# Kernel tuning notes

Hardware: AMD Instinct MI355X
Metric: run time of the kernel (lower is better)

Reference implementation:

```python
import jax, jax.numpy as jnp
import numpy as np

EPS = 1e-15
BN_EPS = 1e-5
N_NODES = 50000
N_EDGES = 800000
IN_CH = 32
OUT_CH = 32
DIM = 3


def _gmm_params(key, in_ch, out_ch, K):
    k1, k2, k3, k4 = jax.random.split(key, 4)
    g = jax.random.normal(k1, (in_ch, K * out_ch), jnp.float32) * (1.0 / np.sqrt(in_ch))
    mu = jax.random.normal(k2, (K, DIM), jnp.float32)
    sigma = jax.random.uniform(k3, (K, DIM), jnp.float32, 0.5, 1.5)
    root = jax.random.normal(k4, (in_ch, out_ch), jnp.float32) * (1.0 / np.sqrt(in_ch))
    bias = jnp.zeros((out_ch,), jnp.float32)
    return g, mu, sigma, root, bias


def setup_inputs() -> dict:
    key = jax.random.key(0)
    ks = jax.random.split(key, 12)
    x = jax.random.normal(ks[0], (N_NODES, IN_CH), jnp.float32)
    edge_index = jax.random.randint(ks[1], (2, N_EDGES), 0, N_NODES, jnp.int64)
    edge_attr = jax.random.uniform(ks[2], (N_EDGES, DIM), jnp.float32)
    g1, mu1, sig1, root1, b1 = _gmm_params(ks[3], IN_CH, OUT_CH, 5)
    g2, mu2, sig2, root2, b2 = _gmm_params(ks[4], OUT_CH, OUT_CH, 5)
    gs, mus, sigs, roots, bs = _gmm_params(ks[5], IN_CH, OUT_CH, 1)
    ones = jnp.ones((OUT_CH,), jnp.float32)
    zeros = jnp.zeros((OUT_CH,), jnp.float32)
    return dict(x=x, edge_attr=edge_attr,
                g1=g1, mu1=mu1, sig1=sig1, root1=root1, b1=b1, gam1=ones, bet1=zeros,
                g2=g2, mu2=mu2, sig2=sig2, root2=root2, b2=b2, gam2=ones, bet2=zeros,
                gs=gs, mus=mus, sigs=sigs, roots=roots, bs=bs, gams=ones, bets=zeros,
                edge_index=edge_index)


def gmm_conv(x, edge_index, edge_attr, g, mu, sigma, root, bias, num_nodes):
    # PyG GMMConv (separate kernels=False, aggr='mean', root_weight=True)
    src, dst = edge_index[0], edge_index[1]
    K = mu.shape[0]
    out_ch = root.shape[1]
    # Gaussian mixture weights per edge/kernel: [E, K]
    diff = edge_attr[:, None, :] - mu[None, :, :]               # [E, K, D]
    w = jnp.exp(jnp.sum(-0.5 * diff * diff / (EPS + sigma[None] ** 2), axis=-1))
    # Project and gather source features: [E, K, out]
    xj = (x @ g).reshape(-1, K, out_ch)[src] if False else (x[src] @ g).reshape(-1, K, out_ch)
    msg = jnp.einsum('ek,ekc->ec', w, xj)                        # [E, out]
    agg = jax.ops.segment_sum(msg, dst, num_segments=num_nodes)
    cnt = jax.ops.segment_sum(jnp.ones((msg.shape[0],), msg.dtype), dst, num_segments=num_nodes)
    agg = agg / jnp.maximum(cnt, 1.0)[:, None]                   # mean aggregation
    return agg + x @ root + bias


def batch_norm(x, gamma, beta):
    mean = jnp.mean(x, axis=0)
    var = jnp.var(x, axis=0)
    return gamma * (x - mean) * jax.lax.rsqrt(var + BN_EPS) + beta


def reference(x, edge_attr,
              g1, mu1, sig1, root1, b1, gam1, bet1,
              g2, mu2, sig2, root2, b2, gam2, bet2,
              gs, mus, sigs, roots, bs, gams, bets,
              edge_index):
    n = x.shape[0]
    h = jax.nn.elu(batch_norm(gmm_conv(x, edge_index, edge_attr, g1, mu1, sig1, root1, b1, n), gam1, bet1))
    h = batch_norm(gmm_conv(h, edge_index, edge_attr, g2, mu2, sig2, root2, b2, n), gam2, bet2)
    s = batch_norm(gmm_conv(x, edge_index, edge_attr, gs, mus, sigs, roots, bs, n), gams, bets)
    return jax.nn.elu(h + s)
```

## Files before the change

kernel.cpp:

```cpp
#include <hip/hip_runtime.h>
#include <hip/hip_fp16.h>
#include <math.h>

#define NN 50000
#define NE 800000
#define GEPS 1e-15f
#define BN_EPS 1e-5f
#define NB 196
#define LOG2E 1.4426950408889634f
#define NODES_PER_XCD 6250

typedef _Float16 f16x8 __attribute__((ext_vector_type(8)));
typedef float f32x4 __attribute__((ext_vector_type(4)));

__device__ __forceinline__ float2 h2f(unsigned int u) {
    __half2 h = *reinterpret_cast<const __half2*>(&u);
    return __half22float2(h);
}

__global__ void init_kernel(const float* __restrict__ sig1, const float* __restrict__ mu1,
                            const float* __restrict__ sig2, const float* __restrict__ mu2,
                            const float* __restrict__ sigs, const float* __restrict__ mus,
                            float* __restrict__ gc, int* __restrict__ deg,
                            float* __restrict__ stats) {
    int i = blockIdx.x * blockDim.x + threadIdx.x;
    if (i < NN) deg[i] = 0;
    if (blockIdx.x == 0) {
        int t = threadIdx.x;
        stats[t] = 0.f;
        if (t < 11) {
            const float* sg; const float* mu;
            if (t < 5)       { sg = sig1 + t * 3;       mu = mu1 + t * 3; }
            else if (t < 10) { sg = sig2 + (t - 5) * 3; mu = mu2 + (t - 5) * 3; }
            else             { sg = sigs;               mu = mus; }
            float C = 0.f;
            for (int d = 0; d < 3; d++) {
                float sv = sg[d];
                float iv = -0.5f / (GEPS + sv * sv) * LOG2E;
                float m = mu[d];
                gc[t * 8 + d] = iv;
                gc[t * 8 + 3 + d] = -2.f * iv * m;
                C += iv * m * m;
            }
            gc[t * 8 + 6] = C;
            gc[t * 8 + 7] = 0.f;
        }
    }
}

__global__ void rank_kernel(const int* __restrict__ ei, int* __restrict__ deg,
                            int* __restrict__ rankv) {
    int t = blockIdx.x * blockDim.x + threadIdx.x;
    int e0 = t * 4;
    if (e0 >= NE) return;
    int4 dv = *(const int4*)(ei + NE + e0);
    int4 rv;
    rv.x = atomicAdd(&deg[dv.x], 1);
    rv.y = atomicAdd(&deg[dv.y], 1);
    rv.z = atomicAdd(&deg[dv.z], 1);
    rv.w = atomicAdd(&deg[dv.w], 1);
    *(int4*)(rankv + e0) = rv;
}

__global__ void block_reduce_kernel(const int* __restrict__ deg, int* __restrict__ bsum) {
    __shared__ int sh[256];
    int t = threadIdx.x;
    int i = blockIdx.x * 256 + t;
    sh[t] = (i < NN) ? deg[i] : 0;
    __syncthreads();
    for (int off = 128; off > 0; off >>= 1) {
        if (t < off) sh[t] += sh[t + off];
        __syncthreads();
    }
    if (t == 0) bsum[blockIdx.x] = sh[0];
}

__global__ void scan_partials_kernel(int* __restrict__ bsum) {
    __shared__ int sh[256];
    int t = threadIdx.x;
    int v = (t < NB) ? bsum[t] : 0;
    sh[t] = v;
    __syncthreads();
    for (int off = 1; off < 256; off <<= 1) {
        int u = (t >= off) ? sh[t - off] : 0;
        __syncthreads();
        sh[t] += u;
        __syncthreads();
    }
    if (t < NB) bsum[t] = sh[t] - v;
}

__global__ void block_scan_kernel(const int* __restrict__ deg, const int* __restrict__ bsum,
                                  int* __restrict__ rowstart) {
    __shared__ int sh[256];
    int t = threadIdx.x;
    int i = blockIdx.x * 256 + t;
    int v = (i < NN) ? deg[i] : 0;
    sh[t] = v;
    __syncthreads();
    for (int off = 1; off < 256; off <<= 1) {
        int u = (t >= off) ? sh[t - off] : 0;
        __syncthreads();
        sh[t] += u;
        __syncthreads();
    }
    int excl = sh[t] - v + bsum[blockIdx.x];
    if (i < NN) rowstart[i] = excl;
}

__global__ void scatter_proj_kernel(const int* __restrict__ ei, const int* __restrict__ rankv,
                                    const int* __restrict__ rowstart, int* __restrict__ perm,
                                    const float* __restrict__ x, const float* __restrict__ root1,
                                    const float* __restrict__ b1, const float* __restrict__ roots,
                                    const float* __restrict__ bs, __half* __restrict__ xh,
                                    float* __restrict__ R1, float* __restrict__ Rs) {
    if (blockIdx.x < 1024) {
        const int g = blockIdx.x & 7;
        const int v = blockIdx.x >> 3;
        const int VB = 1024 >> 3;
        const int stride = VB * blockDim.x * 4;
        for (int e0 = (v * blockDim.x + threadIdx.x) * 4; e0 < NE; e0 += stride) {
            int4 dv = *(const int4*)(ei + NE + e0);
            int4 rv = *(const int4*)(rankv + e0);
            if (dv.x / NODES_PER_XCD == g) perm[rowstart[dv.x] + rv.x] = e0;
            if (dv.y / NODES_PER_XCD == g) perm[rowstart[dv.y] + rv.y] = e0 + 1;
            if (dv.z / NODES_PER_XCD == g) perm[rowstart[dv.z] + rv.z] = e0 + 2;
            if (dv.w / NODES_PER_XCD == g) perm[rowstart[dv.w] + rv.w] = e0 + 3;
        }
    } else {
        const int pb = blockIdx.x - 1024;
        const int t = threadIdx.x;
        const int col = t & 31;
        const int half_ = (t >> 5) & 1;
        const int rg = t >> 6;
        float w[32];
        const float* rootp = half_ ? roots : root1;
#pragma unroll
        for (int i = 0; i < 32; i++) w[i] = rootp[i * 32 + col];
        float b = half_ ? bs[col] : b1[col];
        float* Rp = half_ ? Rs : R1;
        __shared__ float hs[256];
        for (int n0 = pb * 8; n0 < NN; n0 += 512 * 8) {
            float v = x[(size_t)n0 * 32 + t];
            hs[t] = v;
            xh[(size_t)n0 * 32 + t] = __float2half(v);
            __syncthreads();
#pragma unroll
            for (int rr = 0; rr < 2; rr++) {
                int r = rg * 2 + rr;
                float acc = b;
#pragma unroll
                for (int i = 0; i < 32; i++) acc += w[i] * hs[r * 32 + i];
                Rp[(size_t)(n0 + r) * 32 + col] = acc;
            }
            __syncthreads();
        }
    }
}

__global__ void reorder_build(const int* __restrict__ perm, const int* __restrict__ ei,
                              const float* __restrict__ ea, const float* __restrict__ gc,
                              int4* __restrict__ recA, int4* __restrict__ recB) {
    int t = blockIdx.x * blockDim.x + threadIdx.x;
    int p0 = t * 4;
    if (p0 >= NE) return;
    int4 pv = *(const int4*)(perm + p0);
    int es[4] = {pv.x, pv.y, pv.z, pv.w};

    int   srcs[4];
    float av[4][3];
#pragma unroll
    for (int k = 0; k < 4; k++) {
        int e = es[k];
        srcs[k] = ei[e];
        av[k][0] = ea[e * 3 + 0];
        av[k][1] = ea[e * 3 + 1];
        av[k][2] = ea[e * 3 + 2];
    }

    int4 qa[4], qb[4];
#pragma unroll
    for (int k = 0; k < 4; k++) {
        float a0 = av[k][0], a1 = av[k][1], a2 = av[k][2];
        float s0 = a0 * a0, s1 = a1 * a1, s2 = a2 * a2;
        __half wv[11];
#pragma unroll
        for (int s = 0; s < 11; s++) {
            float ex = gc[s * 8 + 6];
            ex = fmaf(gc[s * 8 + 3], a0, ex);
            ex = fmaf(gc[s * 8 + 4], a1, ex);
            ex = fmaf(gc[s * 8 + 5], a2, ex);
            ex = fmaf(gc[s * 8 + 0], s0, ex);
            ex = fmaf(gc[s * 8 + 1], s1, ex);
            ex = fmaf(gc[s * 8 + 2], s2, ex);
            wv[s] = __float2half(exp2f(ex));
        }
        union UA { struct { int src; __half w[6]; } r; int4 q; } ua;
        ua.r.src = srcs[k];
        ua.r.w[0] = wv[0]; ua.r.w[1] = wv[1]; ua.r.w[2] = wv[2];
        ua.r.w[3] = wv[3]; ua.r.w[4] = wv[4]; ua.r.w[5] = wv[10];
        union UB { struct { int src; __half w[5]; __half pad; } r; int4 q; } ub;
        ub.r.src = srcs[k];
        ub.r.w[0] = wv[5]; ub.r.w[1] = wv[6]; ub.r.w[2] = wv[7];
        ub.r.w[3] = wv[8]; ub.r.w[4] = wv[9]; ub.r.pad = __float2half(0.f);
        qa[k] = ua.q;
        qb[k] = ub.q;
    }
#pragma unroll
    for (int k = 0; k < 4; k++) recA[p0 + k] = qa[k];
#pragma unroll
    for (int k = 0; k < 4; k++) recB[p0 + k] = qb[k];
}

__global__ void projB2_kernel(const float* __restrict__ c1, const float* __restrict__ stats,
                              const float* __restrict__ gam1, const float* __restrict__ bet1,
                              const float* __restrict__ root2, const float* __restrict__ b2,
                              __half* __restrict__ hh, float* __restrict__ R2) {
    const int t = threadIdx.x;
    const int col = t & 31;
    const int rg = t >> 5;
    __shared__ float sc[32], sf[32];
    if (t < 32) {
        const float invN = 1.0f / (float)NN;
        float m = stats[t] * invN;
        float v = stats[32 + t] * invN - m * m;
        float s = gam1[t] * rsqrtf(v + BN_EPS);
        sc[t] = s;
        sf[t] = bet1[t] - m * s;
    }
    float w[32];
#pragma unroll
    for (int i = 0; i < 32; i++) w[i] = root2[i * 32 + col];
    float b = b2[col];
    __shared__ float hs[256];
    __syncthreads();
    for (int n0 = blockIdx.x * 8; n0 < NN; n0 += gridDim.x * 8) {
        float v = c1[(size_t)n0 * 32 + t];
        float hv = sc[t & 31] * v + sf[t & 31];
        hv = hv > 0.f ? hv : (__expf(hv) - 1.f);
        hs[t] = hv;
        hh[(size_t)n0 * 32 + t] = __float2half(hv);
        __syncthreads();
        float acc = b;
#pragma unroll
        for (int i = 0; i < 32; i++) acc += w[i] * hs[rg * 32 + i];
        R2[(size_t)(n0 + rg) * 32 + col] = acc;
        __syncthreads();
    }
}

template <bool SKIP>
__global__ void agg_kernel(const int4* __restrict__ rec, const int* __restrict__ rowstart,
                           const int* __restrict__ deg, const __half* __restrict__ X,
                           __half* __restrict__ Aout) {
    constexpr int NS = SKIP ? 6 : 5;
    constexpr int SA = SKIP ? 192 : 160;
    const int tid = blockIdx.x * blockDim.x + threadIdx.x;
    const int lane = threadIdx.x & 63;
    const int grp = lane >> 4;
    const int ch2 = lane & 15;
    const int wavesTotal = (gridDim.x * blockDim.x) >> 6;
    const int wid = tid >> 6;

    for (int n = wid; n < NN; n += wavesTotal) {
        const int start = rowstart[n];
        const int d = deg[n];
        float2 acc[NS];
#pragma unroll
        for (int s = 0; s < NS; s++) acc[s] = make_float2(0.f, 0.f);
        int i = grp;
        for (; i + 4 < d; i += 8) {
            int4 r0 = rec[(size_t)(start + i)];
            int4 r1 = rec[(size_t)(start + i + 4)];
            const __half2 xv0 = *(const __half2*)(X + (((size_t)r0.x) << 5) + 2 * ch2);
            const __half2 xv1 = *(const __half2*)(X + (((size_t)r1.x) << 5) + 2 * ch2);
            float2 xf0 = __half22float2(xv0);
            float2 xf1 = __half22float2(xv1);
            {
                float2 w01 = h2f((unsigned)r0.y);
                float2 w23 = h2f((unsigned)r0.z);
                float2 w45 = h2f((unsigned)r0.w);
                float wv[6] = {w01.x, w01.y, w23.x, w23.y, w45.x, w45.y};
#pragma unroll
                for (int s = 0; s < NS; s++) {
                    acc[s].x = fmaf(wv[s], xf0.x, acc[s].x);
                    acc[s].y = fmaf(wv[s], xf0.y, acc[s].y);
                }
            }
            {
                float2 w01 = h2f((unsigned)r1.y);
                float2 w23 = h2f((unsigned)r1.z);
                float2 w45 = h2f((unsigned)r1.w);
                float wv[6] = {w01.x, w01.y, w23.x, w23.y, w45.x, w45.y};
#pragma unroll
                for (int s = 0; s < NS; s++) {
                    acc[s].x = fmaf(wv[s], xf1.x, acc[s].x);
                    acc[s].y = fmaf(wv[s], xf1.y, acc[s].y);
                }
            }
        }
        if (i < d) {
            int4 r = rec[(size_t)(start + i)];
            const __half2 xv = *(const __half2*)(X + (((size_t)r.x) << 5) + 2 * ch2);
            float2 xf = __half22float2(xv);
            float2 w01 = h2f((unsigned)r.y);
            float2 w23 = h2f((unsigned)r.z);
            float2 w45 = h2f((unsigned)r.w);
            float wv[6] = {w01.x, w01.y, w23.x, w23.y, w45.x, w45.y};
#pragma unroll
            for (int s = 0; s < NS; s++) {
                acc[s].x = fmaf(wv[s], xf.x, acc[s].x);
                acc[s].y = fmaf(wv[s], xf.y, acc[s].y);
            }
        }
#pragma unroll
        for (int s = 0; s < NS; s++) {
            acc[s].x += __shfl_xor(acc[s].x, 16, 64);
            acc[s].x += __shfl_xor(acc[s].x, 32, 64);
            acc[s].y += __shfl_xor(acc[s].y, 16, 64);
            acc[s].y += __shfl_xor(acc[s].y, 32, 64);
        }
        if (grp == 0) {
            const float invd = 1.0f / fmaxf((float)d, 1.0f);
            __half* base = Aout + (size_t)n * SA + 2 * ch2;
#pragma unroll
            for (int s = 0; s < 5; s++) {
                __half2 hv = __floats2half2_rn(acc[s].x * invd, acc[s].y * invd);
                *(__half2*)(base + s * 32) = hv;
            }
            if (SKIP) {
                __half2 hv = __floats2half2_rn(acc[5].x * invd, acc[5].y * invd);
                *(__half2*)(base + 160) = hv;
            }
        }
    }
}

template <bool SKIP>
__global__ __launch_bounds__(256, 4) void gemm_kernel(
        const __half* __restrict__ Ah, const float* __restrict__ G,
        const float* __restrict__ Gs, const float* __restrict__ R,
        const float* __restrict__ Rs, float* __restrict__ C,
        float* __restrict__ Cs, float* __restrict__ stats) {
    constexpr int SA = SKIP ? 192 : 160;
    const int tid = blockIdx.x * blockDim.x + threadIdx.x;
    const int l = threadIdx.x & 63;
    const int r16 = l & 15;
    const int quad = l >> 4;
    const int wid = tid >> 6;
    const int nw = (gridDim.x * blockDim.x) >> 6;

    f16x8 bf[5][2];
#pragma unroll
    for (int kt = 0; kt < 5; kt++)
#pragma unroll
        for (int ct = 0; ct < 2; ct++)
#pragma unroll
            for (int e = 0; e < 8; e++) {
                int jj = quad * 8 + e;
                bf[kt][ct][e] = (_Float16)G[jj * 160 + kt * 32 + ct * 16 + r16];
            }
    f16x8 bs[2];
    if (SKIP) {
#pragma unroll
        for (int ct = 0; ct < 2; ct++)
#pragma unroll
            for (int e = 0; e < 8; e++) {
                int jj = quad * 8 + e;
                bs[ct][e] = (_Float16)Gs[jj * 32 + ct * 16 + r16];
            }
    }

    float s0 = 0.f, s1 = 0.f, q0 = 0.f, q1 = 0.f;
    float t0 = 0.f, t1 = 0.f, u0 = 0.f, u1 = 0.f;

    for (int tile = wid; tile < NN / 16; tile += nw) {
        const int n0 = tile * 16;
        const __half* arow = Ah + (size_t)(n0 + r16) * SA + quad * 8;
        f32x4 acc0 = {0.f, 0.f, 0.f, 0.f};
        f32x4 acc1 = {0.f, 0.f, 0.f, 0.f};
        f32x4 sa0 = {0.f, 0.f, 0.f, 0.f};
        f32x4 sa1 = {0.f, 0.f, 0.f, 0.f};
#pragma unroll
        for (int kt = 0; kt < 5; kt++) {
            f16x8 a = *(const f16x8*)(arow + kt * 32);
            acc0 = __builtin_amdgcn_mfma_f32_16x16x32_f16(a, bf[kt][0], acc0, 0, 0, 0);
            acc1 = __builtin_amdgcn_mfma_f32_16x16x32_f16(a, bf[kt][1], acc1, 0, 0, 0);
        }
        if (SKIP) {
            f16x8 a = *(const f16x8*)(arow + 160);
            sa0 = __builtin_amdgcn_mfma_f32_16x16x32_f16(a, bs[0], sa0, 0, 0, 0);
            sa1 = __builtin_amdgcn_mfma_f32_16x16x32_f16(a, bs[1], sa1, 0, 0, 0);
        }
#pragma unroll
        for (int r = 0; r < 4; r++) {
            const int nr = n0 + quad * 4 + r;
            const int b = nr * 32;
            {
                float v = acc0[r] + R[b + r16];
                C[b + r16] = v; s0 += v; q0 += v * v;
            }
            {
                float v = acc1[r] + R[b + 16 + r16];
                C[b + 16 + r16] = v; s1 += v; q1 += v * v;
            }
            if (SKIP) {
                float v = sa0[r] + Rs[b + r16];
                Cs[b + r16] = v; t0 += v; u0 += v * v;
                float w2 = sa1[r] + Rs[b + 16 + r16];
                Cs[b + 16 + r16] = w2; t1 += w2; u1 += w2 * w2;
            }
        }
    }
    s0 += __shfl_xor(s0, 16, 64); s0 += __shfl_xor(s0, 32, 64);
    s1 += __shfl_xor(s1, 16, 64); s1 += __shfl_xor(s1, 32, 64);
    q0 += __shfl_xor(q0, 16, 64); q0 += __shfl_xor(q0, 32, 64);
    q1 += __shfl_xor(q1, 16, 64); q1 += __shfl_xor(q1, 32, 64);
    if (SKIP) {
        t0 += __shfl_xor(t0, 16, 64); t0 += __shfl_xor(t0, 32, 64);
        t1 += __shfl_xor(t1, 16, 64); t1 += __shfl_xor(t1, 32, 64);
        u0 += __shfl_xor(u0, 16, 64); u0 += __shfl_xor(u0, 32, 64);
        u1 += __shfl_xor(u1, 16, 64); u1 += __shfl_xor(u1, 32, 64);
    }
    __shared__ float sred[128];
    const int t = threadIdx.x;
    if (t < 128) sred[t] = 0.f;
    __syncthreads();
    if (l < 16) {
        atomicAdd(&sred[l], s0);       atomicAdd(&sred[16 + l], s1);
        atomicAdd(&sred[32 + l], q0);  atomicAdd(&sred[48 + l], q1);
        if (SKIP) {
            atomicAdd(&sred[64 + l], t0);  atomicAdd(&sred[80 + l], t1);
            atomicAdd(&sred[96 + l], u0);  atomicAdd(&sred[112 + l], u1);
        }
    }
    __syncthreads();
    if (SKIP) { if (t < 128) atomicAdd(&stats[t], sred[t]); }
    else      { if (t < 64)  atomicAdd(&stats[t], sred[t]); }
}

__global__ void apply2_kernel(const float* __restrict__ c2, const float* __restrict__ cs,
                              const float* __restrict__ stats, const float* __restrict__ gam2,
                              const float* __restrict__ bet2, const float* __restrict__ gams,
                              const float* __restrict__ bets, float* __restrict__ out) {
    int idx = blockIdx.x * blockDim.x + threadIdx.x;
    if (idx >= NN * 32) return;
    int ch = idx & 31;
    const float invN = 1.0f / (float)NN;
    float m2 = stats[128 + ch] * invN;
    float v2 = stats[160 + ch] * invN - m2 * m2;
    float ms = stats[64 + ch] * invN;
    float vs = stats[96 + ch] * invN - ms * ms;
    float bn2 = gam2[ch] * (c2[idx] - m2) * rsqrtf(v2 + BN_EPS) + bet2[ch];
    float bns = gams[ch] * (cs[idx] - ms) * rsqrtf(vs + BN_EPS) + bets[ch];
    float o = bn2 + bns;
    out[idx] = o > 0.f ? o : (__expf(o) - 1.f);
}

extern "C" void kernel_launch(void* const* d_in, const int* in_sizes, int n_in,
                              void* d_out, int out_size, void* d_ws, size_t ws_size,
                              hipStream_t stream) {
    const float* x     = (const float*)d_in[0];
    const float* ea    = (const float*)d_in[1];
    const float* g1    = (const float*)d_in[2];
    const float* mu1   = (const float*)d_in[3];
    const float* sig1  = (const float*)d_in[4];
    const float* root1 = (const float*)d_in[5];
    const float* b1    = (const float*)d_in[6];
    const float* gam1  = (const float*)d_in[7];
    const float* bet1  = (const float*)d_in[8];
    const float* g2    = (const float*)d_in[9];
    const float* mu2   = (const float*)d_in[10];
    const float* sig2  = (const float*)d_in[11];
    const float* root2 = (const float*)d_in[12];
    const float* b2    = (const float*)d_in[13];
    const float* gam2  = (const float*)d_in[14];
    const float* bet2  = (const float*)d_in[15];
    const float* gs    = (const float*)d_in[16];
    const float* mus   = (const float*)d_in[17];
    const float* sigs  = (const float*)d_in[18];
    const float* roots = (const float*)d_in[19];
    const float* bs    = (const float*)d_in[20];
    const float* gams  = (const float*)d_in[21];
    const float* bets  = (const float*)d_in[22];
    const int*   ei    = (const int*)d_in[23];
    float* out = (float*)d_out;

    char* w = (char*)d_ws;
    __half* xh  = (__half*)w;   w += (size_t)NN * 32 * 2;
    __half* hh  = (__half*)w;   w += (size_t)NN * 32 * 2;
    __half* Ah  = (__half*)w;   w += (size_t)NN * 192 * 2;
    float*  R1  = (float*)w;    w += (size_t)NN * 32 * 4;
    float*  Rs  = (float*)w;    w += (size_t)NN * 32 * 4;
    float*  R2  = (float*)w;    w += (size_t)NN * 32 * 4;
    float*  c1  = (float*)w;    w += (size_t)NN * 32 * 4;
    float*  cs  = (float*)w;    w += (size_t)NN * 32 * 4;
    int4*   recA = (int4*)w;    w += (size_t)NE * 16;
    int4*   recB = (int4*)w;    w += (size_t)NE * 16;
    int*    perm = (int*)w;     w += (size_t)NE * 4;
    int*    rankv = (int*)w;    w += (size_t)NE * 4;
    int*    deg = (int*)w;      w += (size_t)NN * 4;
    int*    rowstart = (int*)w; w += (size_t)NN * 4;
    int*    bsum = (int*)w;     w += 256 * 4;
    float*  stats = (float*)w;  w += 256 * 4;
    float*  gc    = (float*)w;  w += 11 * 8 * 4;

    const int ilpBlocks   = (NE / 4 + 255) / 256;
    const int applyBlocks = (NN * 32 + 255) / 256;

    init_kernel<<<NB, 256, 0, stream>>>(sig1, mu1, sig2, mu2, sigs, mus, gc, deg, stats);

    rank_kernel<<<ilpBlocks, 256, 0, stream>>>(ei, deg, rankv);
    block_reduce_kernel<<<NB, 256, 0, stream>>>(deg, bsum);
    scan_partials_kernel<<<1, 256, 0, stream>>>(bsum);
    block_scan_kernel<<<NB, 256, 0, stream>>>(deg, bsum, rowstart);
    scatter_proj_kernel<<<1536, 256, 0, stream>>>(ei, rankv, rowstart, perm,
                                                  x, root1, b1, roots, bs, xh, R1, Rs);
    reorder_build<<<ilpBlocks, 256, 0, stream>>>(perm, ei, ea, gc, recA, recB);

    agg_kernel<true><<<2048, 256, 0, stream>>>(recA, rowstart, deg, xh, Ah);
    gemm_kernel<true><<<512, 256, 0, stream>>>(Ah, g1, gs, R1, Rs, c1, cs, stats);

    projB2_kernel<<<1024, 256, 0, stream>>>(c1, stats, gam1, bet1, root2, b2, hh, R2);
    agg_kernel<false><<<2048, 256, 0, stream>>>(recB, rowstart, deg, hh, Ah);
    gemm_kernel<false><<<512, 256, 0, stream>>>(Ah, g2, nullptr, R2, nullptr, c1, nullptr,
                                                stats + 128);
    apply2_kernel<<<applyBlocks, 256, 0, stream>>>(c1, cs, stats, gam2, bet2, gams, bets, out);
}
```

Before: 294.3 us.

## Split edge-record build and overlap recB construction with layer-1 aggregation

The record-build kernel is split so that only the layer-1/skip records (recA) are built before the first aggregation. The layer-2 records (recB) are now built by extra blocks appended to the layer-1 aggregation launch, so that compute-heavy exp work can overlap with the memory-bound gather. The aggregation body is factored into a shared device function. The risk is that the build blocks compete for CU resources with the aggregation waves, and the grid-stride agg loop now uses a fixed AGG_BLOCKS count.

```diff
diff --git a/kernel.cpp b/kernel.cpp
--- a/kernel.cpp
+++ b/kernel.cpp
@@ -9,6 +9,8 @@
 #define NB 196
 #define LOG2E 1.4426950408889634f
 #define NODES_PER_XCD 6250
+#define AGG_BLOCKS 2048
+#define BUILD_BLOCKS 782
 
 typedef _Float16 f16x8 __attribute__((ext_vector_type(8)));
 typedef float f32x4 __attribute__((ext_vector_type(4)));
@@ -158,9 +160,9 @@
     }
 }
 
-__global__ void reorder_build(const int* __restrict__ perm, const int* __restrict__ ei,
+__global__ void buildA_kernel(const int* __restrict__ perm, const int* __restrict__ ei,
                               const float* __restrict__ ea, const float* __restrict__ gc,
-                              int4* __restrict__ recA, int4* __restrict__ recB) {
+                              int4* __restrict__ recA) {
     int t = blockIdx.x * blockDim.x + threadIdx.x;
     int p0 = t * 4;
     if (p0 >= NE) return;
@@ -178,14 +180,15 @@
         av[k][2] = ea[e * 3 + 2];
     }
 
-    int4 qa[4], qb[4];
+    int4 qa[4];
 #pragma unroll
     for (int k = 0; k < 4; k++) {
         float a0 = av[k][0], a1 = av[k][1], a2 = av[k][2];
         float s0 = a0 * a0, s1 = a1 * a1, s2 = a2 * a2;
-        __half wv[11];
-#pragma unroll
-        for (int s = 0; s < 11; s++) {
+        __half wv[6];
+#pragma unroll
+        for (int si = 0; si < 6; si++) {
+            int s = (si < 5) ? si : 10;
             float ex = gc[s * 8 + 6];
             ex = fmaf(gc[s * 8 + 3], a0, ex);
             ex = fmaf(gc[s * 8 + 4], a1, ex);
@@ -193,23 +196,16 @@
             ex = fmaf(gc[s * 8 + 0], s0, ex);
             ex = fmaf(gc[s * 8 + 1], s1, ex);
             ex = fmaf(gc[s * 8 + 2], s2, ex);
-            wv[s] = __float2half(exp2f(ex));
+            wv[si] = __float2half(exp2f(ex));
         }
         union UA { struct { int src; __half w[6]; } r; int4 q; } ua;
         ua.r.src = srcs[k];
         ua.r.w[0] = wv[0]; ua.r.w[1] = wv[1]; ua.r.w[2] = wv[2];
-        ua.r.w[3] = wv[3]; ua.r.w[4] = wv[4]; ua.r.w[5] = wv[10];
-        union UB { struct { int src; __half w[5]; __half pad; } r; int4 q; } ub;
-        ub.r.src = srcs[k];
-        ub.r.w[0] = wv[5]; ub.r.w[1] = wv[6]; ub.r.w[2] = wv[7];
-        ub.r.w[3] = wv[8]; ub.r.w[4] = wv[9]; ub.r.pad = __float2half(0.f);
+        ua.r.w[3] = wv[3]; ua.r.w[4] = wv[4]; ua.r.w[5] = wv[5];
         qa[k] = ua.q;
-        qb[k] = ub.q;
     }
 #pragma unroll
     for (int k = 0; k < 4; k++) recA[p0 + k] = qa[k];
-#pragma unroll
-    for (int k = 0; k < 4; k++) recB[p0 + k] = qb[k];
 }
 
 __global__ void projB2_kernel(const float* __restrict__ c1, const float* __restrict__ stats,
@@ -249,90 +245,151 @@
     }
 }
 
-template <bool SKIP>
-__global__ void agg_kernel(const int4* __restrict__ rec, const int* __restrict__ rowstart,
-                           const int* __restrict__ deg, const __half* __restrict__ X,
-                           __half* __restrict__ Aout) {
-    constexpr int NS = SKIP ? 6 : 5;
-    constexpr int SA = SKIP ? 192 : 160;
+template <int NS, int SA>
+__device__ __forceinline__ void agg_node_body(
+        const int4* __restrict__ rec, const __half* __restrict__ X,
+        __half* __restrict__ Aout, int n, int start, int d, int grp, int ch2) {
+    float2 acc[NS];
+#pragma unroll
+    for (int s = 0; s < NS; s++) acc[s] = make_float2(0.f, 0.f);
+    int i = grp;
+    for (; i + 4 < d; i += 8) {
+        int4 r0 = rec[(size_t)(start + i)];
+        int4 r1 = rec[(size_t)(start + i + 4)];
+        const __half2 xv0 = *(const __half2*)(X + (((size_t)r0.x) << 5) + 2 * ch2);
+        const __half2 xv1 = *(const __half2*)(X + (((size_t)r1.x) << 5) + 2 * ch2);
+        float2 xf0 = __half22float2(xv0);
+        float2 xf1 = __half22float2(xv1);
+        {
+            float2 w01 = h2f((unsigned)r0.y);
+            float2 w23 = h2f((unsigned)r0.z);
+            float2 w45 = h2f((unsigned)r0.w);
+            float wv[6] = {w01.x, w01.y, w23.x, w23.y, w45.x, w45.y};
+#pragma unroll
+            for (int s = 0; s < NS; s++) {
+                acc[s].x = fmaf(wv[s], xf0.x, acc[s].x);
+                acc[s].y = fmaf(wv[s], xf0.y, acc[s].y);
+            }
+        }
+        {
+            float2 w01 = h2f((unsigned)r1.y);
+            float2 w23 = h2f((unsigned)r1.z);
+            float2 w45 = h2f((unsigned)r1.w);
+            float wv[6] = {w01.x, w01.y, w23.x, w23.y, w45.x, w45.y};
+#pragma unroll
+            for (int s = 0; s < NS; s++) {
+                acc[s].x = fmaf(wv[s], xf1.x, acc[s].x);
+                acc[s].y = fmaf(wv[s], xf1.y, acc[s].y);
+            }
+        }
+    }
+    if (i < d) {
+        int4 r = rec[(size_t)(start + i)];
+        const __half2 xv = *(const __half2*)(X + (((size_t)r.x) << 5) + 2 * ch2);
+        float2 xf = __half22float2(xv);
+        float2 w01 = h2f((unsigned)r.y);
+        float2 w23 = h2f((unsigned)r.z);
+        float2 w45 = h2f((unsigned)r.w);
+        float wv[6] = {w01.x, w01.y, w23.x, w23.y, w45.x, w45.y};
+#pragma unroll
+        for (int s = 0; s < NS; s++) {
+            acc[s].x = fmaf(wv[s], xf.x, acc[s].x);
+            acc[s].y = fmaf(wv[s], xf.y, acc[s].y);
+        }
+    }
+#pragma unroll
+    for (int s = 0; s < NS; s++) {
+        acc[s].x += __shfl_xor(acc[s].x, 16, 64);
+        acc[s].x += __shfl_xor(acc[s].x, 32, 64);
+        acc[s].y += __shfl_xor(acc[s].y, 16, 64);
+        acc[s].y += __shfl_xor(acc[s].y, 32, 64);
+    }
+    if (grp == 0) {
+        const float invd = 1.0f / fmaxf((float)d, 1.0f);
+        __half* base = Aout + (size_t)n * SA + 2 * ch2;
+#pragma unroll
+        for (int s = 0; s < 5; s++) {
+            __half2 hv = __floats2half2_rn(acc[s].x * invd, acc[s].y * invd);
+            *(__half2*)(base + s * 32) = hv;
+        }
+        if (NS == 6) {
+            __half2 hv = __floats2half2_rn(acc[5].x * invd, acc[5].y * invd);
+            *(__half2*)(base + 160) = hv;
+        }
+    }
+}
+
+__global__ void aggA_buildB_kernel(const int4* __restrict__ recA, const int* __restrict__ rowstart,
+                                   const int* __restrict__ deg, const __half* __restrict__ X,
+                                   __half* __restrict__ Aout, const int* __restrict__ perm,
+                                   const int* __restrict__ ei, const float* __restrict__ ea,
+                                   const float* __restrict__ gc, int4* __restrict__ recB) {
+    if (blockIdx.x < AGG_BLOCKS) {
+        const int tid = blockIdx.x * blockDim.x + threadIdx.x;
+        const int lane = threadIdx.x & 63;
+        const int grp = lane >> 4;
+        const int ch2 = lane & 15;
+        const int wavesTotal = (AGG_BLOCKS * 256) >> 6;
+        const int wid = tid >> 6;
+        for (int n = wid; n < NN; n += wavesTotal) {
+            agg_node_body<6, 192>(recA, X, Aout, n, rowstart[n], deg[n], grp, ch2);
+        }
+    } else {
+        int t = (blockIdx.x - AGG_BLOCKS) * blockDim.x + threadIdx.x;
+        int p0 = t * 4;
+        if (p0 >= NE) return;
+        int4 pv = *(const int4*)(perm + p0);
+        int es[4] = {pv.x, pv.y, pv.z, pv.w};
+        int   srcs[4];
+        float av[4][3];
+#pragma unroll
+        for (int k = 0; k < 4; k++) {
+            int e = es[k];
+            srcs[k] = ei[e];
+            av[k][0] = ea[e * 3 + 0];
+            av[k][1] = ea[e * 3 + 1];
+            av[k][2] = ea[e * 3 + 2];
+        }
+        int4 qb[4];
+#pragma unroll
+        for (int k = 0; k < 4; k++) {
+            float a0 = av[k][0], a1 = av[k][1], a2 = av[k][2];
+            float s0 = a0 * a0, s1 = a1 * a1, s2 = a2 * a2;
+            __half wv[5];
+#pragma unroll
+            for (int si = 0; si < 5; si++) {
+                int s = 5 + si;
+                float ex = gc[s * 8 + 6];
+                ex = fmaf(gc[s * 8 + 3], a0, ex);
+                ex = fmaf(gc[s * 8 + 4], a1, ex);
+                ex = fmaf(gc[s * 8 + 5], a2, ex);
+                ex = fmaf(gc[s * 8 + 0], s0, ex);
+                ex = fmaf(gc[s * 8 + 1], s1, ex);
+                ex = fmaf(gc[s * 8 + 2], s2, ex);
+                wv[si] = __float2half(exp2f(ex));
+            }
+            union UB { struct { int src; __half w[5]; __half pad; } r; int4 q; } ub;
+            ub.r.src = srcs[k];
+            ub.r.w[0] = wv[0]; ub.r.w[1] = wv[1]; ub.r.w[2] = wv[2];
+            ub.r.w[3] = wv[3]; ub.r.w[4] = wv[4]; ub.r.pad = __float2half(0.f);
+            qb[k] = ub.q;
+        }
+#pragma unroll
+        for (int k = 0; k < 4; k++) recB[p0 + k] = qb[k];
+    }
+}
+
+__global__ void aggB_kernel(const int4* __restrict__ rec, const int* __restrict__ rowstart,
+                            const int* __restrict__ deg, const __half* __restrict__ X,
+                            __half* __restrict__ Aout) {
     const int tid = blockIdx.x * blockDim.x + threadIdx.x;
     const int lane = threadIdx.x & 63;
     const int grp = lane >> 4;
     const int ch2 = lane & 15;
     const int wavesTotal = (gridDim.x * blockDim.x) >> 6;
     const int wid = tid >> 6;
-
     for (int n = wid; n < NN; n += wavesTotal) {
-        const int start = rowstart[n];
-        const int d = deg[n];
-        float2 acc[NS];
-#pragma unroll
-        for (int s = 0; s < NS; s++) acc[s] = make_float2(0.f, 0.f);
-        int i = grp;
-        for (; i + 4 < d; i += 8) {
-            int4 r0 = rec[(size_t)(start + i)];
-            int4 r1 = rec[(size_t)(start + i + 4)];
-            const __half2 xv0 = *(const __half2*)(X + (((size_t)r0.x) << 5) + 2 * ch2);
-            const __half2 xv1 = *(const __half2*)(X + (((size_t)r1.x) << 5) + 2 * ch2);
-            float2 xf0 = __half22float2(xv0);
-            float2 xf1 = __half22float2(xv1);
-            {
-                float2 w01 = h2f((unsigned)r0.y);
-                float2 w23 = h2f((unsigned)r0.z);
-                float2 w45 = h2f((unsigned)r0.w);
-                float wv[6] = {w01.x, w01.y, w23.x, w23.y, w45.x, w45.y};
-#pragma unroll
-                for (int s = 0; s < NS; s++) {
-                    acc[s].x = fmaf(wv[s], xf0.x, acc[s].x);
-                    acc[s].y = fmaf(wv[s], xf0.y, acc[s].y);
-                }
-            }
-            {
-                float2 w01 = h2f((unsigned)r1.y);
-                float2 w23 = h2f((unsigned)r1.z);
-                float2 w45 = h2f((unsigned)r1.w);
-                float wv[6] = {w01.x, w01.y, w23.x, w23.y, w45.x, w45.y};
-#pragma unroll
-                for (int s = 0; s < NS; s++) {
-                    acc[s].x = fmaf(wv[s], xf1.x, acc[s].x);
-                    acc[s].y = fmaf(wv[s], xf1.y, acc[s].y);
-                }
-            }
-        }
-        if (i < d) {
-            int4 r = rec[(size_t)(start + i)];
-            const __half2 xv = *(const __half2*)(X + (((size_t)r.x) << 5) + 2 * ch2);
-            float2 xf = __half22float2(xv);
-            float2 w01 = h2f((unsigned)r.y);
-            float2 w23 = h2f((unsigned)r.z);
-            float2 w45 = h2f((unsigned)r.w);
-            float wv[6] = {w01.x, w01.y, w23.x, w23.y, w45.x, w45.y};
-#pragma unroll
-            for (int s = 0; s < NS; s++) {
-                acc[s].x = fmaf(wv[s], xf.x, acc[s].x);
-                acc[s].y = fmaf(wv[s], xf.y, acc[s].y);
-            }
-        }
-#pragma unroll
-        for (int s = 0; s < NS; s++) {
-            acc[s].x += __shfl_xor(acc[s].x, 16, 64);
-            acc[s].x += __shfl_xor(acc[s].x, 32, 64);
-            acc[s].y += __shfl_xor(acc[s].y, 16, 64);
-            acc[s].y += __shfl_xor(acc[s].y, 32, 64);
-        }
-        if (grp == 0) {
-            const float invd = 1.0f / fmaxf((float)d, 1.0f);
-            __half* base = Aout + (size_t)n * SA + 2 * ch2;
-#pragma unroll
-            for (int s = 0; s < 5; s++) {
-                __half2 hv = __floats2half2_rn(acc[s].x * invd, acc[s].y * invd);
-                *(__half2*)(base + s * 32) = hv;
-            }
-            if (SKIP) {
-                __half2 hv = __floats2half2_rn(acc[5].x * invd, acc[5].y * invd);
-                *(__half2*)(base + 160) = hv;
-            }
-        }
+        agg_node_body<5, 160>(rec, X, Aout, n, rowstart[n], deg[n], grp, ch2);
     }
 }
 
@@ -516,13 +573,14 @@
     block_scan_kernel<<<NB, 256, 0, stream>>>(deg, bsum, rowstart);
     scatter_proj_kernel<<<1536, 256, 0, stream>>>(ei, rankv, rowstart, perm,
                                                   x, root1, b1, roots, bs, xh, R1, Rs);
-    reorder_build<<<ilpBlocks, 256, 0, stream>>>(perm, ei, ea, gc, recA, recB);
-
-    agg_kernel<true><<<2048, 256, 0, stream>>>(recA, rowstart, deg, xh, Ah);
+    buildA_kernel<<<ilpBlocks, 256, 0, stream>>>(perm, ei, ea, gc, recA);
+
+    aggA_buildB_kernel<<<AGG_BLOCKS + BUILD_BLOCKS, 256, 0, stream>>>(
+        recA, rowstart, deg, xh, Ah, perm, ei, ea, gc, recB);
     gemm_kernel<true><<<512, 256, 0, stream>>>(Ah, g1, gs, R1, Rs, c1, cs, stats);
 
     projB2_kernel<<<1024, 256, 0, stream>>>(c1, stats, gam1, bet1, root2, b2, hh, R2);
-    agg_kernel<false><<<2048, 256, 0, stream>>>(recB, rowstart, deg, hh, Ah);
+    aggB_kernel<<<2048, 256, 0, stream>>>(recB, rowstart, deg, hh, Ah);
     gemm_kernel<false><<<512, 256, 0, stream>>>(Ah, g2, nullptr, R2, nullptr, c1, nullptr,
                                                 stats + 128);
     apply2_kernel<<<applyBlocks, 256, 0, stream>>>(c1, cs, stats, gam2, bet2, gams, bets, out);
```

Result: slower. 312.8 us (+6.3%).
